# Kernel tuning notes

Measured on AMD Instinct MI355X. Metric: run time of the kernel, lower is better.

The kernel has to match this reference:

```python
import jax, jax.numpy as jnp
import numpy as np

# geomloss SamplesLoss('sinkhorn', p=2, blur=0.05, diameter=4.0, scaling=0.5, debias=True)
P_EXP = 2.0
BLUR = 0.05
DIAMETER = 4.0
SCALING = 0.5


def eps_schedule():
    # geomloss epsilon_schedule: annealed temperatures from diameter^p down to blur^p
    mids = [np.exp(e) for e in np.arange(P_EXP * np.log(DIAMETER), P_EXP * np.log(BLUR), P_EXP * np.log(SCALING))]
    return [float(DIAMETER ** P_EXP)] + [float(e) for e in mids] + [float(BLUR ** P_EXP)]


def sq_cost(x, y):
    # C[b,i,j] = 0.5 * ||x_bi - y_bj||^2   (geomloss p=2 cost)
    x2 = jnp.sum(x * x, axis=-1)[:, :, None]   # [B,N,1]
    y2 = jnp.sum(y * y, axis=-1)[:, None, :]   # [B,1,M]
    return 0.5 * (x2 + y2) - jnp.einsum('bid,bjd->bij', x, y)


def softmin(eps, C, h):
    # h: [B,M] dual log-potential; C: [B,N,M] -> [B,N]
    return -eps * jax.nn.logsumexp(h[:, None, :] - C / eps, axis=2)


def sinkhorn_divergence(x, y):
    B, N, _ = x.shape
    M = y.shape[1]
    dt = x.dtype
    a_log = jnp.full((B, N), -np.log(N), dtype=dt)  # uniform weights (log)
    b_log = jnp.full((B, M), -np.log(M), dtype=dt)

    C_xy = sq_cost(x, y)
    C_yx = sq_cost(y, x)
    C_xx = sq_cost(x, x)
    C_yy = sq_cost(y, y)

    eps_list = eps_schedule()
    eps = eps_list[0]
    # initialization (damping = 1 for balanced OT)
    a_x = softmin(eps, C_xx, a_log)
    b_y = softmin(eps, C_yy, b_log)
    b_x = softmin(eps, C_xy, b_log)
    a_y = softmin(eps, C_yx, a_log)

    # eps-scaling descent with symmetrized updates (runs under no_grad in geomloss)
    for eps in eps_list:
        at_y = softmin(eps, C_yx, a_log + b_x / eps)
        bt_x = softmin(eps, C_xy, b_log + a_y / eps)
        at_x = softmin(eps, C_xx, a_log + a_x / eps)
        bt_y = softmin(eps, C_yy, b_log + b_y / eps)
        a_y, b_x = 0.5 * (a_y + at_y), 0.5 * (b_x + bt_x)
        a_x, b_y = 0.5 * (a_x + at_x), 0.5 * (b_y + bt_y)

    # last extrapolation: gradients flow only through the cost matrices here
    eps = eps_list[-1]
    sg = jax.lax.stop_gradient
    a_y, b_x = (softmin(eps, C_yx, sg(a_log + b_x / eps)),
                softmin(eps, C_xy, sg(b_log + a_y / eps)))
    a_x = softmin(eps, C_xx, sg(a_log + a_x / eps))
    b_y = softmin(eps, C_yy, sg(b_log + b_y / eps))

    a = jnp.exp(a_log)
    b = jnp.exp(b_log)
    # debiased Sinkhorn cost per batch, then torch.sum over batch as in forward()
    F = jnp.sum(a * (b_x - a_x), axis=-1) + jnp.sum(b * (a_y - b_y), axis=-1)
    return jnp.sum(F)


def setup_inputs() -> dict:
    key = jax.random.key(0)
    k1, k2 = jax.random.split(key)
    true_data = jax.random.normal(k1, (2, 4096, 3), dtype=jnp.float32)
    particles = jax.random.normal(k2, (2, 4096, 3), dtype=jnp.float32)
    return {"true_data": true_data, "particles": particles}


def reference(true_data, particles):
    # rm_map is identity here: y = rm_map(particles) = particles
    return sinkhorn_divergence(true_data, particles)
```

## Files before the change

kernel.cpp:

```cpp
#include <hip/hip_runtime.h>


typedef __attribute__((ext_vector_type(8))) short short8;
typedef __attribute__((ext_vector_type(8))) __bf16 bf16x8;
typedef __attribute__((ext_vector_type(4))) float f32x4;
typedef __attribute__((ext_vector_type(2))) float f32x2;

#define NPT 4096
#define BLOCK 512
#define COLS 1024
#define NPARTS 4
#define ROWS_PER_BLOCK 256
#define NRC 16
#define EXP2 __builtin_amdgcn_exp2f
#define LOG2 __builtin_amdgcn_logf
#define KLOG2E 1.4426950408889634f
#define KLN2 0.6931471805599453f

__device__ inline unsigned short f2bf(float f) {
  unsigned u = __float_as_uint(f);
  return (unsigned short)((u + 0x7FFF + ((u >> 16) & 1)) >> 16);
}
__device__ inline float bf2f(unsigned short h) {
  return __uint_as_float(((unsigned)h) << 16);
}

struct SArgs {
  const float* rowPts[4];
  const float* colPts[4];
  const float2* Pprev;
  float2* Pcur;
  const float* Fprev;
  float* Fcur;
  float eps, epsPrev;
  int usePot, avgPrev;
};

__device__ inline void lse_merge16(float& m, float& s,
                                   f32x4 c0, f32x4 c1, f32x4 c2, f32x4 c3) {
  float t0 = fmaxf(fmaxf(c0.x, c0.y), c0.z);
  float t1 = fmaxf(fmaxf(c0.w, c1.x), c1.y);
  float t2 = fmaxf(fmaxf(c1.z, c1.w), c2.x);
  float t3 = fmaxf(fmaxf(c2.y, c2.z), c2.w);
  float t4 = fmaxf(fmaxf(c3.x, c3.y), c3.z);
  float u0 = fmaxf(fmaxf(t0, t1), c3.w);
  float u1 = fmaxf(fmaxf(t2, t3), t4);
  float cm = fmaxf(u0, u1);
  float mn = fmaxf(m, cm);
  float sc = EXP2(m - mn);
  f32x2 mn2 = {mn, mn};
  f32x2 sa = {0.0f, 0.0f}, sb = {0.0f, 0.0f};
  f32x2 d;
  d = (f32x2){c0.x, c0.y} - mn2; sa += (f32x2){EXP2(d.x), EXP2(d.y)};
  d = (f32x2){c0.z, c0.w} - mn2; sb += (f32x2){EXP2(d.x), EXP2(d.y)};
  d = (f32x2){c1.x, c1.y} - mn2; sa += (f32x2){EXP2(d.x), EXP2(d.y)};
  d = (f32x2){c1.z, c1.w} - mn2; sb += (f32x2){EXP2(d.x), EXP2(d.y)};
  d = (f32x2){c2.x, c2.y} - mn2; sa += (f32x2){EXP2(d.x), EXP2(d.y)};
  d = (f32x2){c2.z, c2.w} - mn2; sb += (f32x2){EXP2(d.x), EXP2(d.y)};
  d = (f32x2){c3.x, c3.y} - mn2; sa += (f32x2){EXP2(d.x), EXP2(d.y)};
  d = (f32x2){c3.z, c3.w} - mn2; sb += (f32x2){EXP2(d.x), EXP2(d.y)};
  sa += sb;
  s = fmaf(s, sc, sa.x + sa.y);
  m = mn;
}

__global__ __launch_bounds__(BLOCK, 4) void softmin_mfma(SArgs A) {
  __shared__ short8 fragA0[COLS];
  __shared__ short8 fragA1[COLS];

  const int bid  = blockIdx.x;
  const int tbl  = bid >> 6;
  const int task = tbl >> 1, batch = tbl & 1;
  const int rem  = bid & 63;
  const int part = rem >> 4;
  const int rc   = rem & 15;

  const float* yp = A.colPts[task] + batch * NPT * 3;
  const float* xp = A.rowPts[task] + batch * NPT * 3;

  const float inv_eps = 1.0f / A.eps;
  const float sY = inv_eps * KLOG2E;
  const float hc = -8.317766166719343f;
  const int pidxA[4] = {1, 0, 2, 3};
  const int tP = pidxA[task] * 2 + batch;

  const int lane = threadIdx.x & 63;
  const int wave = threadIdx.x >> 6;
  const int q    = lane >> 4;

  const int rowbase = rc * ROWS_PER_BLOCK + wave * 32;
  bf16x8 Bf[2];
#pragma unroll
  for (int rs = 0; rs < 2; ++rs) {
    int i = rowbase + rs * 16 + (lane & 15);
    float X0 = xp[3 * i], X1 = xp[3 * i + 1], X2 = xp[3 * i + 2];
    unsigned short xh0 = f2bf(X0), xh1 = f2bf(X1), xh2 = f2bf(X2);
    unsigned short xl0 = f2bf(X0 - bf2f(xh0));
    unsigned short xl1 = f2bf(X1 - bf2f(xh1));
    unsigned short xl2 = f2bf(X2 - bf2f(xh2));
    short8 bb = (short8)0;
    if (q == 0) {
      short8 t = {(short)xh0, (short)xh1, (short)xh2,
                  (short)xh0, (short)xh1, (short)xh2,
                  (short)xl0, (short)xl1};
      bb = t;
    } else if (q == 1) {
      short8 t = {(short)xl2, (short)0x3F80, (short)0x3F80, (short)0x3F80,
                  (short)xl0, (short)xl1, (short)xl2, 0};
      bb = t;
    }
    Bf[rs] = __builtin_bit_cast(bf16x8, bb);
  }

  for (int c = 0; c < COLS / BLOCK; ++c) {
    int jl = threadIdx.x + c * BLOCK;
    int j  = part * COLS + jl;
    float y0 = yp[3 * j], y1 = yp[3 * j + 1], y2 = yp[3 * j + 2];
    float y2n = 0.5f * (y0 * y0 + y1 * y1 + y2 * y2);
    float pot = 0.0f;
    if (A.usePot) {
      float2 q0 = A.Pprev[(tP * 4 + 0) * NPT + j];
      float2 q1 = A.Pprev[(tP * 4 + 1) * NPT + j];
      float2 q2 = A.Pprev[(tP * 4 + 2) * NPT + j];
      float2 q3 = A.Pprev[(tP * 4 + 3) * NPT + j];
      float M = fmaxf(fmaxf(q0.x, q1.x), fmaxf(q2.x, q3.x));
      float S = q0.y * EXP2(q0.x - M) + q1.y * EXP2(q1.x - M)
              + q2.y * EXP2(q2.x - M) + q3.y * EXP2(q3.x - M);
      float L = M + LOG2(S);
      float r = y2n - A.epsPrev * KLN2 * L;
      if (A.avgPrev) r = 0.5f * (A.Fprev[tP * NPT + j] + r);
      pot = r;
      if (rc == 0) A.Fcur[tP * NPT + j] = pot;
    }
    float T = (hc + (pot - y2n) * inv_eps) * KLOG2E;
    float s0 = y0 * sY, s1 = y1 * sY, s2 = y2 * sY;
    unsigned short yh0 = f2bf(s0), yh1 = f2bf(s1), yh2 = f2bf(s2);
    unsigned short yl0 = f2bf(s0 - bf2f(yh0));
    unsigned short yl1 = f2bf(s1 - bf2f(yh1));
    unsigned short yl2 = f2bf(s2 - bf2f(yh2));
    unsigned short Th = f2bf(T);
    float tr = T - bf2f(Th);
    unsigned short Tm = f2bf(tr);
    tr -= bf2f(Tm);
    unsigned short Tl = f2bf(tr);
    short8 h0 = {(short)yh0, (short)yh1, (short)yh2,
                 (short)yl0, (short)yl1, (short)yl2,
                 (short)yh0, (short)yh1};
    short8 h1 = {(short)yh2, (short)Th, (short)Tm, (short)Tl,
                 (short)yl0, (short)yl1, (short)yl2, 0};
    fragA0[jl] = h0;
    fragA1[jl] = h1;
  }
  __syncthreads();

  const short8* srcA = (lane & 16) ? fragA1 : fragA0;
  const int colsel = lane & 15;
  const f32x4 Z = {0.0f, 0.0f, 0.0f, 0.0f};
  short8 as0 = (short8)0, as1 = (short8)0, as2 = (short8)0, as3 = (short8)0;
  float m0 = -__builtin_inff(), s0_ = 0.0f;
  float m1 = -__builtin_inff(), s1_ = 0.0f;

  for (int jt = 0; jt < COLS / 16; jt += 4) {
    if (lane < 32) {
      as0 = srcA[(jt + 0) * 16 + colsel];
      as1 = srcA[(jt + 1) * 16 + colsel];
      as2 = srcA[(jt + 2) * 16 + colsel];
      as3 = srcA[(jt + 3) * 16 + colsel];
    }
    bf16x8 A0 = __builtin_bit_cast(bf16x8, as0);
    bf16x8 A1 = __builtin_bit_cast(bf16x8, as1);
    bf16x8 A2 = __builtin_bit_cast(bf16x8, as2);
    bf16x8 A3 = __builtin_bit_cast(bf16x8, as3);
    f32x4 c00 = __builtin_amdgcn_mfma_f32_16x16x32_bf16(A0, Bf[0], Z, 0, 0, 0);
    f32x4 c01 = __builtin_amdgcn_mfma_f32_16x16x32_bf16(A1, Bf[0], Z, 0, 0, 0);
    f32x4 c02 = __builtin_amdgcn_mfma_f32_16x16x32_bf16(A2, Bf[0], Z, 0, 0, 0);
    f32x4 c03 = __builtin_amdgcn_mfma_f32_16x16x32_bf16(A3, Bf[0], Z, 0, 0, 0);
    f32x4 c10 = __builtin_amdgcn_mfma_f32_16x16x32_bf16(A0, Bf[1], Z, 0, 0, 0);
    f32x4 c11 = __builtin_amdgcn_mfma_f32_16x16x32_bf16(A1, Bf[1], Z, 0, 0, 0);
    f32x4 c12 = __builtin_amdgcn_mfma_f32_16x16x32_bf16(A2, Bf[1], Z, 0, 0, 0);
    f32x4 c13 = __builtin_amdgcn_mfma_f32_16x16x32_bf16(A3, Bf[1], Z, 0, 0, 0);
    lse_merge16(m0, s0_, c00, c01, c02, c03);
    lse_merge16(m1, s1_, c10, c11, c12, c13);
  }

#pragma unroll
  for (int rs = 0; rs < 2; ++rs) {
    float m = rs ? m1 : m0;
    float s = rs ? s1_ : s0_;
#pragma unroll
    for (int off = 16; off <= 32; off <<= 1) {
      float mo = __shfl_xor(m, off, 64);
      float so = __shfl_xor(s, off, 64);
      float mn = fmaxf(m, mo);
      s = s * EXP2(m - mn) + so * EXP2(mo - mn);
      m = mn;
    }
    if (lane < 16) {
      int i = rowbase + rs * 16 + lane;
      A.Pcur[(tbl * 4 + part) * NPT + i] = make_float2(m, s);
    }
  }
}

__global__ __launch_bounds__(256) void reduce1(const float2* P, float* R1) {
  int u = blockIdx.x * 256 + threadIdx.x;
  int b = u >> 12, i = u & 4095;
  float Ls[4];
#pragma unroll
  for (int t = 0; t < 4; ++t) {
    int tbl = t * 2 + b;
    float2 q0 = P[(tbl * 4 + 0) * NPT + i];
    float2 q1 = P[(tbl * 4 + 1) * NPT + i];
    float2 q2 = P[(tbl * 4 + 2) * NPT + i];
    float2 q3 = P[(tbl * 4 + 3) * NPT + i];
    float M = fmaxf(fmaxf(q0.x, q1.x), fmaxf(q2.x, q3.x));
    float S = q0.y * EXP2(q0.x - M) + q1.y * EXP2(q1.x - M)
            + q2.y * EXP2(q2.x - M) + q3.y * EXP2(q3.x - M);
    Ls[t] = M + LOG2(S);
  }
  float acc = (Ls[0] - Ls[2]) + (Ls[1] - Ls[3]);
#pragma unroll
  for (int off = 32; off >= 1; off >>= 1) acc += __shfl_xor(acc, off, 64);
  __shared__ float red[4];
  int wave = threadIdx.x >> 6, lane = threadIdx.x & 63;
  if (lane == 0) red[wave] = acc;
  __syncthreads();
  if (threadIdx.x == 0)
    R1[blockIdx.x] = red[0] + red[1] + red[2] + red[3];
}

__global__ __launch_bounds__(64) void reduce2(const float* R1, float* out) {
  float a = (threadIdx.x < 32) ? R1[threadIdx.x] : 0.0f;
#pragma unroll
  for (int off = 32; off >= 1; off >>= 1) a += __shfl_xor(a, off, 64);
  if (threadIdx.x == 0)
    out[0] = a * (-0.0025f * KLN2 / 4096.0f);
}

extern "C" void kernel_launch(void* const* d_in, const int* in_sizes, int n_in,
                              void* d_out, int out_size, void* d_ws, size_t ws_size,
                              hipStream_t stream) {
  const float* x = (const float*)d_in[0];
  const float* y = (const float*)d_in[1];
  float* out = (float*)d_out;
  float* W = (float*)d_ws;

  float2* P[2] = { (float2*)W, (float2*)(W + 262144) };
  float*  F[2] = { W + 524288, W + 557056 };
  float*  R1buf = W + 589824;

  static const float epsL[11] = {16.0f, 16.0f, 16.0f, 4.0f, 1.0f, 0.25f, 0.0625f,
                                 0.015625f, 0.00390625f, 0.0025f, 0.0025f};
  static const int avgL[11] = {0, 1, 1, 1, 1, 1, 1, 1, 1, 1, 0};

  const float* rows[4] = { x, y, x, y };
  const float* cols[4] = { y, x, x, y };

  dim3 grid(8 * NPARTS * NRC), block(BLOCK);
  for (int L = 0; L <= 10; ++L) {
    SArgs A;
    for (int t = 0; t < 4; ++t) { A.rowPts[t] = rows[t]; A.colPts[t] = cols[t]; }
    A.Pprev = P[(L + 1) & 1];
    A.Pcur  = P[L & 1];
    A.Fprev = F[(L + 1) & 1];
    A.Fcur  = F[L & 1];
    A.eps = epsL[L];
    A.epsPrev = (L > 0) ? epsL[L - 1] : 1.0f;
    A.usePot = (L > 0) ? 1 : 0;
    A.avgPrev = (L > 0) ? avgL[L - 1] : 0;
    softmin_mfma<<<grid, block, 0, stream>>>(A);
  }
  reduce1<<<32, 256, 0, stream>>>(P[0], R1buf);
  reduce2<<<1, 64, 0, stream>>>(R1buf, out);
}
```

Measured before the change: 321.6 us.

## Fuse eleven softmin launches into one persistent kernel with grid barriers

Replaces the eleven per-epsilon kernel launches with a single persistent kernel of 512 blocks. The blocks loop over the epsilon schedule and synchronise through an atomic-counter grid barrier, and the column point coordinates and squared norms are loaded into registers once instead of every launch. This removes launch gaps and repeated setup, but adds spin-wait barrier overhead. It also relies on all 512 blocks being co-resident, and the barrier has a spin timeout that could silently break correctness if they are not.

```diff
diff --git a/kernel.cpp b/kernel.cpp
--- a/kernel.cpp
+++ b/kernel.cpp
@@ -9,14 +9,16 @@
 #define NPT 4096
 #define BLOCK 512
 #define COLS 1024
-#define NPARTS 4
-#define ROWS_PER_BLOCK 256
-#define NRC 16
+#define GRID 512
+#define NLAUNCH 11
 #define EXP2 __builtin_amdgcn_exp2f
 #define LOG2 __builtin_amdgcn_logf
 #define KLOG2E 1.4426950408889634f
 #define KLN2 0.6931471805599453f
 
+__device__ const float epsC[NLAUNCH] = {16.0f, 16.0f, 16.0f, 4.0f, 1.0f, 0.25f,
+                                        0.0625f, 0.015625f, 0.00390625f, 0.0025f, 0.0025f};
+
 __device__ inline unsigned short f2bf(float f) {
   unsigned u = __float_as_uint(f);
   return (unsigned short)((u + 0x7FFF + ((u >> 16) & 1)) >> 16);
@@ -25,16 +27,30 @@
   return __uint_as_float(((unsigned)h) << 16);
 }
 
-struct SArgs {
-  const float* rowPts[4];
-  const float* colPts[4];
-  const float2* Pprev;
-  float2* Pcur;
-  const float* Fprev;
-  float* Fcur;
-  float eps, epsPrev;
-  int usePot, avgPrev;
+struct PArgs {
+  const float* x;
+  const float* y;
+  float2* P0;
+  float2* P1;
+  float* F0;
+  float* F1;
+  unsigned* bar;
 };
+
+__device__ inline void grid_barrier(unsigned* bar, unsigned target) {
+  __syncthreads();
+  if (threadIdx.x == 0) {
+    __threadfence();
+    atomicAdd(bar, 1u);
+    unsigned spins = 0;
+    while (__hip_atomic_load(bar, __ATOMIC_RELAXED, __HIP_MEMORY_SCOPE_AGENT) < target) {
+      __builtin_amdgcn_s_sleep(8);
+      if (++spins > (1u << 22)) break;
+    }
+    __threadfence();
+  }
+  __syncthreads();
+}
 
 __device__ inline void lse_merge16(float& m, float& s,
                                    f32x4 c0, f32x4 c1, f32x4 c2, f32x4 c3) {
@@ -64,7 +80,7 @@
   m = mn;
 }
 
-__global__ __launch_bounds__(BLOCK, 4) void softmin_mfma(SArgs A) {
+__global__ __launch_bounds__(BLOCK, 4) void softmin_persist(PArgs A) {
   __shared__ short8 fragA0[COLS];
   __shared__ short8 fragA1[COLS];
 
@@ -75,11 +91,11 @@
   const int part = rem >> 4;
   const int rc   = rem & 15;
 
-  const float* yp = A.colPts[task] + batch * NPT * 3;
-  const float* xp = A.rowPts[task] + batch * NPT * 3;
-
-  const float inv_eps = 1.0f / A.eps;
-  const float sY = inv_eps * KLOG2E;
+  const bool rowIsX = (task == 0) | (task == 2);
+  const bool colIsX = (task == 1) | (task == 2);
+  const float* xp = (rowIsX ? A.x : A.y) + batch * NPT * 3;
+  const float* yp = (colIsX ? A.x : A.y) + batch * NPT * 3;
+
   const float hc = -8.317766166719343f;
   const int pidxA[4] = {1, 0, 2, 3};
   const int tP = pidxA[task] * 2 + batch;
@@ -87,8 +103,8 @@
   const int lane = threadIdx.x & 63;
   const int wave = threadIdx.x >> 6;
   const int q    = lane >> 4;
-
-  const int rowbase = rc * ROWS_PER_BLOCK + wave * 32;
+  const int rowbase = rc * 256 + wave * 32;
+
   bf16x8 Bf[2];
 #pragma unroll
   for (int rs = 0; rs < 2; ++rs) {
@@ -112,93 +128,119 @@
     Bf[rs] = __builtin_bit_cast(bf16x8, bb);
   }
 
-  for (int c = 0; c < COLS / BLOCK; ++c) {
-    int jl = threadIdx.x + c * BLOCK;
-    int j  = part * COLS + jl;
-    float y0 = yp[3 * j], y1 = yp[3 * j + 1], y2 = yp[3 * j + 2];
-    float y2n = 0.5f * (y0 * y0 + y1 * y1 + y2 * y2);
-    float pot = 0.0f;
-    if (A.usePot) {
-      float2 q0 = A.Pprev[(tP * 4 + 0) * NPT + j];
-      float2 q1 = A.Pprev[(tP * 4 + 1) * NPT + j];
-      float2 q2 = A.Pprev[(tP * 4 + 2) * NPT + j];
-      float2 q3 = A.Pprev[(tP * 4 + 3) * NPT + j];
-      float M = fmaxf(fmaxf(q0.x, q1.x), fmaxf(q2.x, q3.x));
-      float S = q0.y * EXP2(q0.x - M) + q1.y * EXP2(q1.x - M)
-              + q2.y * EXP2(q2.x - M) + q3.y * EXP2(q3.x - M);
-      float L = M + LOG2(S);
-      float r = y2n - A.epsPrev * KLN2 * L;
-      if (A.avgPrev) r = 0.5f * (A.Fprev[tP * NPT + j] + r);
-      pot = r;
-      if (rc == 0) A.Fcur[tP * NPT + j] = pot;
-    }
-    float T = (hc + (pot - y2n) * inv_eps) * KLOG2E;
-    float s0 = y0 * sY, s1 = y1 * sY, s2 = y2 * sY;
-    unsigned short yh0 = f2bf(s0), yh1 = f2bf(s1), yh2 = f2bf(s2);
-    unsigned short yl0 = f2bf(s0 - bf2f(yh0));
-    unsigned short yl1 = f2bf(s1 - bf2f(yh1));
-    unsigned short yl2 = f2bf(s2 - bf2f(yh2));
-    unsigned short Th = f2bf(T);
-    float tr = T - bf2f(Th);
-    unsigned short Tm = f2bf(tr);
-    tr -= bf2f(Tm);
-    unsigned short Tl = f2bf(tr);
-    short8 h0 = {(short)yh0, (short)yh1, (short)yh2,
-                 (short)yl0, (short)yl1, (short)yl2,
-                 (short)yh0, (short)yh1};
-    short8 h1 = {(short)yh2, (short)Th, (short)Tm, (short)Tl,
-                 (short)yl0, (short)yl1, (short)yl2, 0};
-    fragA0[jl] = h0;
-    fragA1[jl] = h1;
-  }
-  __syncthreads();
-
-  const short8* srcA = (lane & 16) ? fragA1 : fragA0;
-  const int colsel = lane & 15;
-  const f32x4 Z = {0.0f, 0.0f, 0.0f, 0.0f};
-  short8 as0 = (short8)0, as1 = (short8)0, as2 = (short8)0, as3 = (short8)0;
-  float m0 = -__builtin_inff(), s0_ = 0.0f;
-  float m1 = -__builtin_inff(), s1_ = 0.0f;
-
-  for (int jt = 0; jt < COLS / 16; jt += 4) {
-    if (lane < 32) {
-      as0 = srcA[(jt + 0) * 16 + colsel];
-      as1 = srcA[(jt + 1) * 16 + colsel];
-      as2 = srcA[(jt + 2) * 16 + colsel];
-      as3 = srcA[(jt + 3) * 16 + colsel];
-    }
-    bf16x8 A0 = __builtin_bit_cast(bf16x8, as0);
-    bf16x8 A1 = __builtin_bit_cast(bf16x8, as1);
-    bf16x8 A2 = __builtin_bit_cast(bf16x8, as2);
-    bf16x8 A3 = __builtin_bit_cast(bf16x8, as3);
-    f32x4 c00 = __builtin_amdgcn_mfma_f32_16x16x32_bf16(A0, Bf[0], Z, 0, 0, 0);
-    f32x4 c01 = __builtin_amdgcn_mfma_f32_16x16x32_bf16(A1, Bf[0], Z, 0, 0, 0);
-    f32x4 c02 = __builtin_amdgcn_mfma_f32_16x16x32_bf16(A2, Bf[0], Z, 0, 0, 0);
-    f32x4 c03 = __builtin_amdgcn_mfma_f32_16x16x32_bf16(A3, Bf[0], Z, 0, 0, 0);
-    f32x4 c10 = __builtin_amdgcn_mfma_f32_16x16x32_bf16(A0, Bf[1], Z, 0, 0, 0);
-    f32x4 c11 = __builtin_amdgcn_mfma_f32_16x16x32_bf16(A1, Bf[1], Z, 0, 0, 0);
-    f32x4 c12 = __builtin_amdgcn_mfma_f32_16x16x32_bf16(A2, Bf[1], Z, 0, 0, 0);
-    f32x4 c13 = __builtin_amdgcn_mfma_f32_16x16x32_bf16(A3, Bf[1], Z, 0, 0, 0);
-    lse_merge16(m0, s0_, c00, c01, c02, c03);
-    lse_merge16(m1, s1_, c10, c11, c12, c13);
-  }
-
-#pragma unroll
-  for (int rs = 0; rs < 2; ++rs) {
-    float m = rs ? m1 : m0;
-    float s = rs ? s1_ : s0_;
-#pragma unroll
-    for (int off = 16; off <= 32; off <<= 1) {
-      float mo = __shfl_xor(m, off, 64);
-      float so = __shfl_xor(s, off, 64);
-      float mn = fmaxf(m, mo);
-      s = s * EXP2(m - mn) + so * EXP2(mo - mn);
-      m = mn;
-    }
-    if (lane < 16) {
-      int i = rowbase + rs * 16 + lane;
-      A.Pcur[(tbl * 4 + part) * NPT + i] = make_float2(m, s);
-    }
+  float Y0[2], Y1[2], Y2[2], Y2N[2];
+#pragma unroll
+  for (int c = 0; c < 2; ++c) {
+    int j = part * COLS + threadIdx.x + c * BLOCK;
+    Y0[c] = yp[3 * j]; Y1[c] = yp[3 * j + 1]; Y2[c] = yp[3 * j + 2];
+    Y2N[c] = 0.5f * (Y0[c] * Y0[c] + Y1[c] * Y1[c] + Y2[c] * Y2[c]);
+  }
+
+  float epsPrev = 1.0f;
+  for (int L = 0; L < NLAUNCH; ++L) {
+    const float eps = epsC[L];
+    const int usePot  = (L >= 1);
+    const int avgPrev = (L >= 2);
+    const float2* Pprev = (L & 1) ? A.P0 : A.P1;
+    float2*       Pcur  = (L & 1) ? A.P1 : A.P0;
+    const float*  Fprev = (L & 1) ? A.F0 : A.F1;
+    float*        Fcur  = (L & 1) ? A.F1 : A.F0;
+    const float inv_eps = 1.0f / eps;
+    const float sY = inv_eps * KLOG2E;
+
+#pragma unroll
+    for (int c = 0; c < 2; ++c) {
+      int jl = threadIdx.x + c * BLOCK;
+      int j  = part * COLS + jl;
+      float y0 = Y0[c], y1 = Y1[c], y2 = Y2[c];
+      float y2n = Y2N[c];
+      float pot = 0.0f;
+      if (usePot) {
+        float2 q0 = Pprev[(tP * 4 + 0) * NPT + j];
+        float2 q1 = Pprev[(tP * 4 + 1) * NPT + j];
+        float2 q2 = Pprev[(tP * 4 + 2) * NPT + j];
+        float2 q3 = Pprev[(tP * 4 + 3) * NPT + j];
+        float M = fmaxf(fmaxf(q0.x, q1.x), fmaxf(q2.x, q3.x));
+        float S = q0.y * EXP2(q0.x - M) + q1.y * EXP2(q1.x - M)
+                + q2.y * EXP2(q2.x - M) + q3.y * EXP2(q3.x - M);
+        float Lg = M + LOG2(S);
+        float r = y2n - epsPrev * KLN2 * Lg;
+        if (avgPrev) r = 0.5f * (Fprev[tP * NPT + j] + r);
+        pot = r;
+        if (rc == 0) Fcur[tP * NPT + j] = pot;
+      }
+      float T = (hc + (pot - y2n) * inv_eps) * KLOG2E;
+      float s0 = y0 * sY, s1 = y1 * sY, s2 = y2 * sY;
+      unsigned short yh0 = f2bf(s0), yh1 = f2bf(s1), yh2 = f2bf(s2);
+      unsigned short yl0 = f2bf(s0 - bf2f(yh0));
+      unsigned short yl1 = f2bf(s1 - bf2f(yh1));
+      unsigned short yl2 = f2bf(s2 - bf2f(yh2));
+      unsigned short Th = f2bf(T);
+      float tr = T - bf2f(Th);
+      unsigned short Tm = f2bf(tr);
+      tr -= bf2f(Tm);
+      unsigned short Tl = f2bf(tr);
+      short8 h0 = {(short)yh0, (short)yh1, (short)yh2,
+                   (short)yl0, (short)yl1, (short)yl2,
+                   (short)yh0, (short)yh1};
+      short8 h1 = {(short)yh2, (short)Th, (short)Tm, (short)Tl,
+                   (short)yl0, (short)yl1, (short)yl2, 0};
+      fragA0[jl] = h0;
+      fragA1[jl] = h1;
+    }
+    __syncthreads();
+
+    const short8* srcA = (lane & 16) ? fragA1 : fragA0;
+    const int colsel = lane & 15;
+    const f32x4 Z = {0.0f, 0.0f, 0.0f, 0.0f};
+    short8 as0 = (short8)0, as1 = (short8)0, as2 = (short8)0, as3 = (short8)0;
+    float m0 = -__builtin_inff(), s0_ = 0.0f;
+    float m1 = -__builtin_inff(), s1_ = 0.0f;
+
+    for (int jt = 0; jt < COLS / 16; jt += 4) {
+      if (lane < 32) {
+        as0 = srcA[(jt + 0) * 16 + colsel];
+        as1 = srcA[(jt + 1) * 16 + colsel];
+        as2 = srcA[(jt + 2) * 16 + colsel];
+        as3 = srcA[(jt + 3) * 16 + colsel];
+      }
+      bf16x8 A0 = __builtin_bit_cast(bf16x8, as0);
+      bf16x8 A1 = __builtin_bit_cast(bf16x8, as1);
+      bf16x8 A2 = __builtin_bit_cast(bf16x8, as2);
+      bf16x8 A3 = __builtin_bit_cast(bf16x8, as3);
+      f32x4 c00 = __builtin_amdgcn_mfma_f32_16x16x32_bf16(A0, Bf[0], Z, 0, 0, 0);
+      f32x4 c01 = __builtin_amdgcn_mfma_f32_16x16x32_bf16(A1, Bf[0], Z, 0, 0, 0);
+      f32x4 c02 = __builtin_amdgcn_mfma_f32_16x16x32_bf16(A2, Bf[0], Z, 0, 0, 0);
+      f32x4 c03 = __builtin_amdgcn_mfma_f32_16x16x32_bf16(A3, Bf[0], Z, 0, 0, 0);
+      f32x4 c10 = __builtin_amdgcn_mfma_f32_16x16x32_bf16(A0, Bf[1], Z, 0, 0, 0);
+      f32x4 c11 = __builtin_amdgcn_mfma_f32_16x16x32_bf16(A1, Bf[1], Z, 0, 0, 0);
+      f32x4 c12 = __builtin_amdgcn_mfma_f32_16x16x32_bf16(A2, Bf[1], Z, 0, 0, 0);
+      f32x4 c13 = __builtin_amdgcn_mfma_f32_16x16x32_bf16(A3, Bf[1], Z, 0, 0, 0);
+      lse_merge16(m0, s0_, c00, c01, c02, c03);
+      lse_merge16(m1, s1_, c10, c11, c12, c13);
+    }
+
+#pragma unroll
+    for (int rs = 0; rs < 2; ++rs) {
+      float m = rs ? m1 : m0;
+      float s = rs ? s1_ : s0_;
+#pragma unroll
+      for (int off = 16; off <= 32; off <<= 1) {
+        float mo = __shfl_xor(m, off, 64);
+        float so = __shfl_xor(s, off, 64);
+        float mn = fmaxf(m, mo);
+        s = s * EXP2(m - mn) + so * EXP2(mo - mn);
+        m = mn;
+      }
+      if (lane < 16) {
+        int i = rowbase + rs * 16 + lane;
+        Pcur[(tbl * 4 + part) * NPT + i] = make_float2(m, s);
+      }
+    }
+
+    epsPrev = eps;
+    if (L < NLAUNCH - 1)
+      grid_barrier(A.bar, (unsigned)(GRID * (L + 1)));
   }
 }
 
@@ -245,31 +287,20 @@
   float* out = (float*)d_out;
   float* W = (float*)d_ws;
 
-  float2* P[2] = { (float2*)W, (float2*)(W + 262144) };
-  float*  F[2] = { W + 524288, W + 557056 };
-  float*  R1buf = W + 589824;
-
-  static const float epsL[11] = {16.0f, 16.0f, 16.0f, 4.0f, 1.0f, 0.25f, 0.0625f,
-                                 0.015625f, 0.00390625f, 0.0025f, 0.0025f};
-  static const int avgL[11] = {0, 1, 1, 1, 1, 1, 1, 1, 1, 1, 0};
-
-  const float* rows[4] = { x, y, x, y };
-  const float* cols[4] = { y, x, x, y };
-
-  dim3 grid(8 * NPARTS * NRC), block(BLOCK);
-  for (int L = 0; L <= 10; ++L) {
-    SArgs A;
-    for (int t = 0; t < 4; ++t) { A.rowPts[t] = rows[t]; A.colPts[t] = cols[t]; }
-    A.Pprev = P[(L + 1) & 1];
-    A.Pcur  = P[L & 1];
-    A.Fprev = F[(L + 1) & 1];
-    A.Fcur  = F[L & 1];
-    A.eps = epsL[L];
-    A.epsPrev = (L > 0) ? epsL[L - 1] : 1.0f;
-    A.usePot = (L > 0) ? 1 : 0;
-    A.avgPrev = (L > 0) ? avgL[L - 1] : 0;
-    softmin_mfma<<<grid, block, 0, stream>>>(A);
-  }
-  reduce1<<<32, 256, 0, stream>>>(P[0], R1buf);
+  PArgs A;
+  A.x = x;
+  A.y = y;
+  A.P0 = (float2*)W;
+  A.P1 = (float2*)(W + 262144);
+  A.F0 = W + 524288;
+  A.F1 = W + 557056;
+  A.bar = (unsigned*)(W + 590080);
+  float* R1buf = W + 589824;
+
+  hipMemsetAsync((void*)A.bar, 0, sizeof(unsigned), stream);
+
+  softmin_persist<<<dim3(GRID), dim3(BLOCK), 0, stream>>>(A);
+
+  reduce1<<<32, 256, 0, stream>>>(A.P0, R1buf);
   reduce2<<<1, 64, 0, stream>>>(R1buf, out);
 }
```

New measurement: 578.0 us. 79.7% more time.
